# Performance work log

Measured on AMD Instinct MI355X. Metric: run time of the kernel, lower is better.

## Reference

```python
import jax, jax.numpy as jnp
import numpy as np

B, H, L, D = 8, 16, 1024, 64

def setup_inputs() -> dict:
    key = jax.random.key(0)
    kq, kk, kv = jax.random.split(key, 3)
    q = jax.random.normal(kq, (B, H, L, D), dtype=jnp.float32)
    k = jax.random.normal(kk, (B, H, L, D), dtype=jnp.float32)
    v = jax.random.normal(kv, (B, H, L, D), dtype=jnp.float32)
    # causal mask, broadcast over batch and head
    mask = jnp.tril(jnp.ones((L, L), dtype=jnp.int32))[None, None, :, :]
    return {"q": q, "k": k, "v": v, "mask": mask}

def reference(q, k, v, mask):
    b, h, l, d = q.shape
    # FAITHFUL to original: k.view(b, h, d, l) is a reshape, NOT a transpose
    k_t = k.reshape(b, h, d, l)
    score = jnp.matmul(q, k_t) / np.sqrt(d).astype(np.float32)  # [b,h,l,l]
    # FAITHFUL to original bug: masked_fill(mask==0, -e) with e=1e-12
    score = jnp.where(mask == 0, jnp.float32(-1e-12), score)
    attn = jax.nn.softmax(score, axis=-1)
    out = jnp.matmul(attn, v)  # [b,h,l,d]
    return (out, attn)
```

## Files before the change

### kernel.cpp

```cpp
#include <hip/hip_runtime.h>

#define L_  1024
#define D_  64
#define TM  128
#define TN  64
#define LDK 72
#define NT  (L_ / TN)

typedef __attribute__((ext_vector_type(8))) short          short8;
typedef __attribute__((ext_vector_type(8))) unsigned short ushort8;
typedef __attribute__((ext_vector_type(4))) float          f32x4;

__device__ __forceinline__ unsigned short bf16r(float f) {
    unsigned u = __builtin_bit_cast(unsigned, f);
    u += 0x7fffu + ((u >> 16) & 1u);
    return (unsigned short)(u >> 16);
}

__global__ __launch_bounds__(256, 2)
void sdpa_kernel(const float* __restrict__ q, const float* __restrict__ kmat,
                 const float* __restrict__ v, float* __restrict__ out,
                 float* __restrict__ attn)
{
    __shared__ __align__(16) unsigned short Qs[TM * LDK];
    __shared__ __align__(16) unsigned short Ks[TN * LDK];
    __shared__ __align__(16) unsigned short Vs[D_ * LDK];
    __shared__ __align__(16) unsigned short Ps[TM * LDK];

    const int t    = threadIdx.x;
    const int wave = t >> 6;
    const int lane = t & 63;
    const int quad = lane >> 4;
    const int l15  = lane & 15;
    const int rt   = blockIdx.x;
    const int bh   = blockIdx.y;
    const int m0   = rt * TM;
    const int rowA = wave * 32;

    const float* qb = q    + (size_t)bh * (L_ * D_);
    const float* kb = kmat + (size_t)bh * (L_ * D_);
    const float* vb = v    + (size_t)bh * (L_ * D_);
    float* outb  = out  + (size_t)bh * (L_ * D_);
    float* attnb = attn + (size_t)bh * ((size_t)L_ * L_);

    #pragma unroll
    for (int i = 0; i < 8; ++i) {
        int idx = (i * 256 + t) * 4;
        int m = idx >> 6, c = idx & 63;
        float4 f = *(const float4*)&qb[(size_t)(m0 + m) * D_ + c];
        ushort4 b;
        b.x = bf16r(f.x); b.y = bf16r(f.y); b.z = bf16r(f.z); b.w = bf16r(f.w);
        *(ushort4*)&Qs[m * LDK + c] = b;
    }

    auto stageK = [&](int nt) {
        const int ng = t & 31, kg = t >> 5;
        const float* src = kb + (size_t)(kg * 8) * L_ + nt * TN + 2 * ng;
        float2 a[8];
        #pragma unroll
        for (int j = 0; j < 8; ++j) a[j] = *(const float2*)(src + (size_t)j * L_);
        ushort8 r0, r1;
        #pragma unroll
        for (int j = 0; j < 8; ++j) { r0[j] = bf16r(a[j].x); r1[j] = bf16r(a[j].y); }
        *(ushort8*)&Ks[(2 * ng)     * LDK + kg * 8] = r0;
        *(ushort8*)&Ks[(2 * ng + 1) * LDK + kg * 8] = r1;
    };
    auto stageV = [&](int nt) {
        const int cg = t & 31, ngp = t >> 5;
        const float* src = vb + (size_t)(nt * TN + ngp * 8) * D_ + 2 * cg;
        float2 a[8];
        #pragma unroll
        for (int j = 0; j < 8; ++j) a[j] = *(const float2*)(src + (size_t)j * D_);
        ushort8 r0, r1;
        #pragma unroll
        for (int j = 0; j < 8; ++j) { r0[j] = bf16r(a[j].x); r1[j] = bf16r(a[j].y); }
        *(ushort8*)&Vs[(2 * cg)     * LDK + ngp * 8] = r0;
        *(ushort8*)&Vs[(2 * cg + 1) * LDK + ngp * 8] = r1;
    };

    auto computeScore = [&](f32x4 (&acc)[2][4]) {
        #pragma unroll
        for (int ks = 0; ks < 2; ++ks) {
            short8 af[2];
            #pragma unroll
            for (int tr = 0; tr < 2; ++tr)
                af[tr] = *(const short8*)&Qs[(rowA + tr * 16 + l15) * LDK + ks * 32 + quad * 8];
            #pragma unroll
            for (int tc = 0; tc < 4; ++tc) {
                short8 bfr = *(const short8*)&Ks[(tc * 16 + l15) * LDK + ks * 32 + quad * 8];
                #pragma unroll
                for (int tr = 0; tr < 2; ++tr)
                    acc[tr][tc] = __builtin_amdgcn_mfma_f32_16x16x32_bf16(af[tr], bfr, acc[tr][tc], 0, 0, 0);
            }
        }
    };

    const f32x4 zero4 = {0.f, 0.f, 0.f, 0.f};

    float zpart[2][4] = {};
    const int ntmax1 = (m0 + TM - 1) / TN;
    __syncthreads();
    for (int nt = 0; nt <= ntmax1; ++nt) {
        stageK(nt);
        __syncthreads();
        f32x4 acc[2][4];
        #pragma unroll
        for (int tr = 0; tr < 2; ++tr)
            #pragma unroll
            for (int tc = 0; tc < 4; ++tc) acc[tr][tc] = zero4;
        computeScore(acc);
        #pragma unroll
        for (int tr = 0; tr < 2; ++tr)
            #pragma unroll
            for (int r = 0; r < 4; ++r) {
                const int gm = m0 + rowA + tr * 16 + quad * 4 + r;
                #pragma unroll
                for (int tc = 0; tc < 4; ++tc) {
                    const int gn = nt * TN + tc * 16 + l15;
                    zpart[tr][r] += (gn > gm) ? 1.0f : __expf(acc[tr][tc][r] * 0.125f);
                }
            }
        __syncthreads();
    }
    const float zmissing = (float)(L_ - (ntmax1 + 1) * TN);
    float rcpz[2][4];
    #pragma unroll
    for (int tr = 0; tr < 2; ++tr)
        #pragma unroll
        for (int r = 0; r < 4; ++r) {
            float z = zpart[tr][r];
            z += __shfl_xor(z, 1);
            z += __shfl_xor(z, 2);
            z += __shfl_xor(z, 4);
            z += __shfl_xor(z, 8);
            rcpz[tr][r] = 1.0f / (z + zmissing);
        }

    f32x4 oacc[2][4];
    #pragma unroll
    for (int tr = 0; tr < 2; ++tr)
        #pragma unroll
        for (int tc = 0; tc < 4; ++tc) oacc[tr][tc] = zero4;

    for (int nt = 0; nt < NT; ++nt) {
        const bool fullmask = (nt * TN) > (m0 + TM - 1);
        __syncthreads();
        if (!fullmask) stageK(nt);
        stageV(nt);
        __syncthreads();

        f32x4 acc[2][4];
        if (!fullmask) {
            #pragma unroll
            for (int tr = 0; tr < 2; ++tr)
                #pragma unroll
                for (int tc = 0; tc < 4; ++tc) acc[tr][tc] = zero4;
            computeScore(acc);
        }

        #pragma unroll
        for (int tr = 0; tr < 2; ++tr)
            #pragma unroll
            for (int r = 0; r < 4; ++r) {
                const int lrow = rowA + tr * 16 + quad * 4 + r;
                const int gm = m0 + lrow;
                #pragma unroll
                for (int tc = 0; tc < 4; ++tc) {
                    const int gn = nt * TN + tc * 16 + l15;
                    float p;
                    if (fullmask) {
                        p = rcpz[tr][r];
                    } else {
                        float e = (gn > gm) ? 1.0f : __expf(acc[tr][tc][r] * 0.125f);
                        p = e * rcpz[tr][r];
                    }
                    attnb[(size_t)gm * L_ + gn] = p;
                    Ps[lrow * LDK + tc * 16 + l15] = bf16r(p);
                }
            }
        __syncthreads();

        #pragma unroll
        for (int ks = 0; ks < 2; ++ks) {
            short8 pf[2];
            #pragma unroll
            for (int tr = 0; tr < 2; ++tr)
                pf[tr] = *(const short8*)&Ps[(rowA + tr * 16 + l15) * LDK + ks * 32 + quad * 8];
            #pragma unroll
            for (int tc = 0; tc < 4; ++tc) {
                short8 vf = *(const short8*)&Vs[(tc * 16 + l15) * LDK + ks * 32 + quad * 8];
                #pragma unroll
                for (int tr = 0; tr < 2; ++tr)
                    oacc[tr][tc] = __builtin_amdgcn_mfma_f32_16x16x32_bf16(pf[tr], vf, oacc[tr][tc], 0, 0, 0);
            }
        }
    }

    #pragma unroll
    for (int tr = 0; tr < 2; ++tr)
        #pragma unroll
        for (int r = 0; r < 4; ++r) {
            const int gm = m0 + rowA + tr * 16 + quad * 4 + r;
            #pragma unroll
            for (int tc = 0; tc < 4; ++tc)
                outb[(size_t)gm * D_ + tc * 16 + l15] = oacc[tr][tc][r];
        }
}

extern "C" void kernel_launch(void* const* d_in, const int* in_sizes, int n_in,
                              void* d_out, int out_size, void* d_ws, size_t ws_size,
                              hipStream_t stream) {
    (void)in_sizes; (void)n_in; (void)d_ws; (void)ws_size; (void)out_size;
    const float* q = (const float*)d_in[0];
    const float* k = (const float*)d_in[1];
    const float* v = (const float*)d_in[2];
    float* out  = (float*)d_out;
    float* attn = (float*)d_out + (size_t)8 * 16 * 1024 * 64;
    dim3 grid(8, 128);
    sdpa_kernel<<<grid, dim3(256), 0, stream>>>(q, k, v, out, attn);
}
```

Measured before the change: 741.1 us.

## Prefetch K/V tiles into registers, swizzle LDS, vectorize masked attn writes

Splits K/V staging into a global load into registers and a later LDS write, so the next tile's global loads are issued before compute on the current tile. The padded LDS layout is replaced by an XOR-swizzled one, which shrinks LDS use and allows occupancy of 3 blocks per CU. Fully masked tiles now write attn and P with float4/ushort4 stores. The barrier before the PV matmul becomes a wave-local lgkmcnt wait, which is valid because each wave reads only its own P rows. In exchange, register pressure rises from holding the prefetched tiles.

```diff
diff --git a/kernel.cpp b/kernel.cpp
--- a/kernel.cpp
+++ b/kernel.cpp
@@ -4,7 +4,6 @@
 #define D_  64
 #define TM  128
 #define TN  64
-#define LDK 72
 #define NT  (L_ / TN)
 
 typedef __attribute__((ext_vector_type(8))) short          short8;
@@ -17,19 +16,23 @@
     return (unsigned short)(u >> 16);
 }
 
-__global__ __launch_bounds__(256, 2)
+__device__ __forceinline__ int swz(int row, int colu) {
+    return row * 64 + ((((colu >> 3) ^ row) & 7) << 3) + (colu & 7);
+}
+
+__global__ __launch_bounds__(256, 3)
 void sdpa_kernel(const float* __restrict__ q, const float* __restrict__ kmat,
                  const float* __restrict__ v, float* __restrict__ out,
                  float* __restrict__ attn)
 {
-    __shared__ __align__(16) unsigned short Qs[TM * LDK];
-    __shared__ __align__(16) unsigned short Ks[TN * LDK];
-    __shared__ __align__(16) unsigned short Vs[D_ * LDK];
-    __shared__ __align__(16) unsigned short Ps[TM * LDK];
+    __shared__ __align__(16) unsigned short Qs[TM * 64];
+    __shared__ __align__(16) unsigned short Ks[TN * 64];
+    __shared__ __align__(16) unsigned short Vs[D_ * 64];
+    __shared__ __align__(16) unsigned short Ps[TM * 64];
 
     const int t    = threadIdx.x;
+    const int lane = t & 63;
     const int wave = t >> 6;
-    const int lane = t & 63;
     const int quad = lane >> 4;
     const int l15  = lane & 15;
     const int rt   = blockIdx.x;
@@ -50,44 +53,48 @@
         float4 f = *(const float4*)&qb[(size_t)(m0 + m) * D_ + c];
         ushort4 b;
         b.x = bf16r(f.x); b.y = bf16r(f.y); b.z = bf16r(f.z); b.w = bf16r(f.w);
-        *(ushort4*)&Qs[m * LDK + c] = b;
+        *(ushort4*)&Qs[swz(m, c)] = b;
     }
 
-    auto stageK = [&](int nt) {
-        const int ng = t & 31, kg = t >> 5;
+    float2 rK[8], rV[8];
+    const int ng = t & 31, kg = t >> 5;
+
+    auto loadK = [&](int nt) {
         const float* src = kb + (size_t)(kg * 8) * L_ + nt * TN + 2 * ng;
-        float2 a[8];
-        #pragma unroll
-        for (int j = 0; j < 8; ++j) a[j] = *(const float2*)(src + (size_t)j * L_);
+        #pragma unroll
+        for (int j = 0; j < 8; ++j) rK[j] = *(const float2*)(src + (size_t)j * L_);
+    };
+    auto writeK = [&]() {
         ushort8 r0, r1;
         #pragma unroll
-        for (int j = 0; j < 8; ++j) { r0[j] = bf16r(a[j].x); r1[j] = bf16r(a[j].y); }
-        *(ushort8*)&Ks[(2 * ng)     * LDK + kg * 8] = r0;
-        *(ushort8*)&Ks[(2 * ng + 1) * LDK + kg * 8] = r1;
-    };
-    auto stageV = [&](int nt) {
-        const int cg = t & 31, ngp = t >> 5;
-        const float* src = vb + (size_t)(nt * TN + ngp * 8) * D_ + 2 * cg;
-        float2 a[8];
-        #pragma unroll
-        for (int j = 0; j < 8; ++j) a[j] = *(const float2*)(src + (size_t)j * D_);
+        for (int j = 0; j < 8; ++j) { r0[j] = bf16r(rK[j].x); r1[j] = bf16r(rK[j].y); }
+        *(ushort8*)&Ks[swz(2 * ng,     kg * 8)] = r0;
+        *(ushort8*)&Ks[swz(2 * ng + 1, kg * 8)] = r1;
+    };
+    auto loadV = [&](int nt) {
+        const float* src = vb + (size_t)(nt * TN + kg * 8) * D_ + 2 * ng;
+        #pragma unroll
+        for (int j = 0; j < 8; ++j) rV[j] = *(const float2*)(src + (size_t)j * D_);
+    };
+    auto writeV = [&]() {
         ushort8 r0, r1;
         #pragma unroll
-        for (int j = 0; j < 8; ++j) { r0[j] = bf16r(a[j].x); r1[j] = bf16r(a[j].y); }
-        *(ushort8*)&Vs[(2 * cg)     * LDK + ngp * 8] = r0;
-        *(ushort8*)&Vs[(2 * cg + 1) * LDK + ngp * 8] = r1;
+        for (int j = 0; j < 8; ++j) { r0[j] = bf16r(rV[j].x); r1[j] = bf16r(rV[j].y); }
+        *(ushort8*)&Vs[swz(2 * ng,     kg * 8)] = r0;
+        *(ushort8*)&Vs[swz(2 * ng + 1, kg * 8)] = r1;
     };
 
     auto computeScore = [&](f32x4 (&acc)[2][4]) {
         #pragma unroll
         for (int ks = 0; ks < 2; ++ks) {
+            const int cu = ks * 32 + quad * 8;
             short8 af[2];
             #pragma unroll
             for (int tr = 0; tr < 2; ++tr)
-                af[tr] = *(const short8*)&Qs[(rowA + tr * 16 + l15) * LDK + ks * 32 + quad * 8];
+                af[tr] = *(const short8*)&Qs[swz(rowA + tr * 16 + l15, cu)];
             #pragma unroll
             for (int tc = 0; tc < 4; ++tc) {
-                short8 bfr = *(const short8*)&Ks[(tc * 16 + l15) * LDK + ks * 32 + quad * 8];
+                short8 bfr = *(const short8*)&Ks[swz(tc * 16 + l15, cu)];
                 #pragma unroll
                 for (int tr = 0; tr < 2; ++tr)
                     acc[tr][tc] = __builtin_amdgcn_mfma_f32_16x16x32_bf16(af[tr], bfr, acc[tr][tc], 0, 0, 0);
@@ -99,9 +106,11 @@
 
     float zpart[2][4] = {};
     const int ntmax1 = (m0 + TM - 1) / TN;
-    __syncthreads();
+    loadK(0);
     for (int nt = 0; nt <= ntmax1; ++nt) {
-        stageK(nt);
+        __syncthreads();
+        writeK();
+        if (nt < ntmax1) loadK(nt + 1);
         __syncthreads();
         f32x4 acc[2][4];
         #pragma unroll
@@ -120,9 +129,12 @@
                     zpart[tr][r] += (gn > gm) ? 1.0f : __expf(acc[tr][tc][r] * 0.125f);
                 }
             }
-        __syncthreads();
     }
     const float zmissing = (float)(L_ - (ntmax1 + 1) * TN);
+
+    loadV(0);
+    loadK(0);
+
     float rcpz[2][4];
     #pragma unroll
     for (int tr = 0; tr < 2; ++tr)
@@ -145,50 +157,66 @@
     for (int nt = 0; nt < NT; ++nt) {
         const bool fullmask = (nt * TN) > (m0 + TM - 1);
         __syncthreads();
-        if (!fullmask) stageK(nt);
-        stageV(nt);
-        __syncthreads();
-
-        f32x4 acc[2][4];
+        writeV();
+        if (!fullmask) writeK();
+        const int nn = nt + 1;
+        if (nn < NT) {
+            loadV(nn);
+            if ((nn * TN) <= (m0 + TM - 1)) loadK(nn);
+        }
+        __syncthreads();
+
         if (!fullmask) {
+            f32x4 acc[2][4];
             #pragma unroll
             for (int tr = 0; tr < 2; ++tr)
                 #pragma unroll
                 for (int tc = 0; tc < 4; ++tc) acc[tr][tc] = zero4;
             computeScore(acc);
-        }
-
-        #pragma unroll
-        for (int tr = 0; tr < 2; ++tr)
-            #pragma unroll
-            for (int r = 0; r < 4; ++r) {
-                const int lrow = rowA + tr * 16 + quad * 4 + r;
-                const int gm = m0 + lrow;
-                #pragma unroll
-                for (int tc = 0; tc < 4; ++tc) {
-                    const int gn = nt * TN + tc * 16 + l15;
-                    float p;
-                    if (fullmask) {
-                        p = rcpz[tr][r];
-                    } else {
+            #pragma unroll
+            for (int tr = 0; tr < 2; ++tr)
+                #pragma unroll
+                for (int r = 0; r < 4; ++r) {
+                    const int lrow = rowA + tr * 16 + quad * 4 + r;
+                    const int gm = m0 + lrow;
+                    #pragma unroll
+                    for (int tc = 0; tc < 4; ++tc) {
+                        const int gn = nt * TN + tc * 16 + l15;
                         float e = (gn > gm) ? 1.0f : __expf(acc[tr][tc][r] * 0.125f);
-                        p = e * rcpz[tr][r];
+                        float p = e * rcpz[tr][r];
+                        attnb[(size_t)gm * L_ + gn] = p;
+                        Ps[swz(lrow, tc * 16 + l15)] = bf16r(p);
                     }
-                    attnb[(size_t)gm * L_ + gn] = p;
-                    Ps[lrow * LDK + tc * 16 + l15] = bf16r(p);
                 }
-            }
-        __syncthreads();
+        } else {
+            #pragma unroll
+            for (int tr = 0; tr < 2; ++tr)
+                #pragma unroll
+                for (int r = 0; r < 4; ++r) {
+                    const int lrow = rowA + tr * 16 + quad * 4 + r;
+                    const int gm = m0 + lrow;
+                    const float rz = rcpz[tr][r];
+                    float4 vv = {rz, rz, rz, rz};
+                    *(float4*)&attnb[(size_t)gm * L_ + nt * TN + 4 * l15] = vv;
+                    const unsigned short pb = bf16r(rz);
+                    ushort4 p4; p4.x = pb; p4.y = pb; p4.z = pb; p4.w = pb;
+                    *(ushort4*)&Ps[swz(lrow, 4 * l15)] = p4;
+                }
+        }
+
+        asm volatile("s_waitcnt lgkmcnt(0)" ::: "memory");
+        __builtin_amdgcn_sched_barrier(0);
 
         #pragma unroll
         for (int ks = 0; ks < 2; ++ks) {
+            const int cu = ks * 32 + quad * 8;
             short8 pf[2];
             #pragma unroll
             for (int tr = 0; tr < 2; ++tr)
-                pf[tr] = *(const short8*)&Ps[(rowA + tr * 16 + l15) * LDK + ks * 32 + quad * 8];
+                pf[tr] = *(const short8*)&Ps[swz(rowA + tr * 16 + l15, cu)];
             #pragma unroll
             for (int tc = 0; tc < 4; ++tc) {
-                short8 vf = *(const short8*)&Vs[(tc * 16 + l15) * LDK + ks * 32 + quad * 8];
+                short8 vf = *(const short8*)&Vs[swz(tc * 16 + l15, cu)];
                 #pragma unroll
                 for (int tr = 0; tr < 2; ++tr)
                     oacc[tr][tc] = __builtin_amdgcn_mfma_f32_16x16x32_bf16(pf[tr], vf, oacc[tr][tc], 0, 0, 0);
```

Measured after the change: 1.075 ms. 45.0% more time.
